# Kernel tuning notes

Hardware: AMD Instinct MI355X
Metric: run time of the kernel (lower is better)

## Reference

```python
import jax, jax.numpy as jnp
import numpy as np

B, D, Q = 256, 2048, 880880
NUM_CLASSES = 1000
T_K = 10.0  # self.T_k


def setup_inputs() -> dict:
    key = jax.random.key(0)
    k1, k2, k3, k4, k5, k6 = jax.random.split(key, 6)
    return {
        "features": jax.random.normal(k1, (B, D), dtype=jnp.float32),
        "labels": jax.random.randint(k2, (B,), 0, NUM_CLASSES),
        "pred": jax.random.randint(k3, (B,), 0, NUM_CLASSES),
        "confidence": jax.random.uniform(k4, (B,), dtype=jnp.float32),
        "queue_mus": jax.random.normal(k5, (Q,), dtype=jnp.float32),
        "queue_sigmas": jax.random.uniform(k6, (Q,), dtype=jnp.float32),
    }


def reference(features, labels, pred, confidence, queue_mus, queue_sigmas):
    # Per-sample feature statistics (torch.std is unbiased -> ddof=1)
    means = jnp.mean(features, axis=1)              # [B]
    stds = jnp.std(features, axis=1, ddof=1)        # [B]
    # Broadcast pairwise 'Wasserstein' distance vs queue: [B, Q]
    wd = jnp.sqrt((means[:, None] - queue_mus[None, :]) ** 2
                  + (stds[:, None] - queue_sigmas[None, :]) ** 2)
    min_distances = jnp.min(wd, axis=1)             # [B]
    # T_scale == 0 branch: T = exp(-T_k * min_dist)
    T = jnp.exp(-T_K * min_distances)
    return T
```

## Files before the change

kernel.cpp:

```cpp
#include <hip/hip_runtime.h>
#include <math.h>

#define NB 256
#define ND 2048
#define T_K 10.0f
#define SCAN2_BLOCKS 512
#define LDSCAP 2048

__global__ __launch_bounds__(256) void stats_probe_kernel(const float* __restrict__ feat,
                                                          const float* __restrict__ mus,
                                                          const float* __restrict__ sigmas,
                                                          float* __restrict__ stats,
                                                          float* __restrict__ u0part,
                                                          int Q) {
    const int b    = blockIdx.x;
    const int tid  = threadIdx.x;
    const int lane = tid & 63, wid = tid >> 6;
    __shared__ float ls[4], lq[4];

    const float4* row = (const float4*)(feat + (size_t)b * ND);
    float sum = 0.f, sumsq = 0.f;
#pragma unroll
    for (int i = 0; i < 2; ++i) {
        float4 v = row[tid + i * 256];
        sum   += v.x + v.y + v.z + v.w;
        sumsq += v.x * v.x + v.y * v.y + v.z * v.z + v.w * v.w;
    }
#pragma unroll
    for (int off = 32; off > 0; off >>= 1) {
        sum   += __shfl_down(sum, off, 64);
        sumsq += __shfl_down(sumsq, off, 64);
    }
    if (lane == 0) { ls[wid] = sum; lq[wid] = sumsq; }
    __syncthreads();
    if (tid == 0) {
        float S  = ls[0] + ls[1] + ls[2] + ls[3];
        float Q2 = lq[0] + lq[1] + lq[2] + lq[3];
        float mean = S / (float)ND;
        float var  = (Q2 - S * mean) / (float)(ND - 1);
        var = fmaxf(var, 0.f);
        stats[b]      = mean;
        stats[NB + b] = sqrtf(var);
    }

    const int nquad = Q >> 2;
    const int chunk = (nquad + NB - 1) / NB;
    const int qs    = b * chunk;
    const int qe    = min(qs + chunk, nquad);
    const float4* mu4 = (const float4*)mus;
    const float4* sg4 = (const float4*)sigmas;

    float best = INFINITY;
    for (int i = qs + tid; i < qe; i += 256) {
        float4 mu = mu4[i], sg = sg4[i];
        float s0 = sg.x - 1.f, s1 = sg.y - 1.f, s2e = sg.z - 1.f, s3 = sg.w - 1.f;
        best = fminf(best, fmaf(mu.x, mu.x, s0 * s0));
        best = fminf(best, fmaf(mu.y, mu.y, s1 * s1));
        best = fminf(best, fmaf(mu.z, mu.z, s2e * s2e));
        best = fminf(best, fmaf(mu.w, mu.w, s3 * s3));
    }
    if (b == 0) {
        int q = nquad * 4 + tid;
        if (q < Q) {
            float dm = mus[q], ds = sigmas[q] - 1.f;
            best = fminf(best, fmaf(dm, dm, ds * ds));
        }
    }
#pragma unroll
    for (int off = 32; off > 0; off >>= 1)
        best = fminf(best, __shfl_down(best, off, 64));
    __syncthreads();
    if (lane == 0) ls[wid] = best;
    __syncthreads();
    if (tid == 0)
        u0part[b] = fminf(fminf(ls[0], ls[1]), fminf(ls[2], ls[3]));
}

__global__ __launch_bounds__(256) void scan_filtered_kernel(const float* __restrict__ mus,
                                                            const float* __restrict__ sigmas,
                                                            const float* __restrict__ stats,
                                                            const float* __restrict__ u0part,
                                                            float* __restrict__ partial,
                                                            int Q) {
    const int tid  = threadIdx.x;
    const int lane = tid & 63, wid = tid >> 6;

    __shared__ float2 buf[LDSCAP];
    __shared__ float  red[4][NB];
    __shared__ float  ls[4], lq[4];
    __shared__ int    cnt;

    float u = u0part[tid];
    float mb = stats[tid], sb = stats[NB + tid];
    float dsb = sb - 1.f;
    float r2 = fmaf(mb, mb, dsb * dsb);
#pragma unroll
    for (int off = 32; off > 0; off >>= 1) {
        u  = fminf(u,  __shfl_down(u,  off, 64));
        r2 = fmaxf(r2, __shfl_down(r2, off, 64));
    }
    if (lane == 0) { ls[wid] = u; lq[wid] = r2; }
    if (tid == 0) cnt = 0;
    __syncthreads();
    const float U0  = fminf(fminf(ls[0], ls[1]), fminf(ls[2], ls[3]));
    const float R2  = fmaxf(fmaxf(lq[0], lq[1]), fmaxf(lq[2], lq[3]));
    const float thr = sqrtf(U0) + 2.f * sqrtf(R2);
    const float thr2 = thr * thr * 1.0001f + 1e-12f;

    float m2[4], s2[4];
#pragma unroll
    for (int k = 0; k < 4; ++k) {
        m2[k] = -2.f * stats[lane + 64 * k];
        s2[k] = -2.f * stats[NB + lane + 64 * k];
    }
    float acc[4];
#pragma unroll
    for (int k = 0; k < 4; ++k) acc[k] = INFINITY;

    const int nquad = Q >> 2;
    const float4* mu4 = (const float4*)mus;
    const float4* sg4 = (const float4*)sigmas;

    for (int cb = blockIdx.x * 256; cb < nquad; cb += SCAN2_BLOCKS * 256) {
        __syncthreads();
        if (cnt > LDSCAP - 1024) {
            const int n = cnt;
            for (int j = wid; j < n; j += 4) {
                float2 p = buf[j];
                float r = fmaf(p.x, p.x, p.y * p.y);
#pragma unroll
                for (int k = 0; k < 4; ++k)
                    acc[k] = fminf(acc[k], fmaf(m2[k], p.x, fmaf(s2[k], p.y, r)));
            }
            __syncthreads();
            if (tid == 0) cnt = 0;
            __syncthreads();
        }
        const int i = cb + tid;
        if (i < nquad) {
            float4 mu = mu4[i], sg = sg4[i];
#define TESTK(MX, SX)                                                        \
            {                                                                \
                float dm = (MX), dss = (SX) - 1.f;                           \
                float dd = fmaf(dm, dm, dss * dss);                          \
                if (dd <= thr2) {                                            \
                    int p = atomicAdd(&cnt, 1);                              \
                    buf[p] = make_float2((MX), (SX));                        \
                }                                                            \
            }
            TESTK(mu.x, sg.x)
            TESTK(mu.y, sg.y)
            TESTK(mu.z, sg.z)
            TESTK(mu.w, sg.w)
        }
    }
    if (blockIdx.x == 0) {
        int q = nquad * 4 + tid;
        if (q < Q) { TESTK(mus[q], sigmas[q]) }
    }
#undef TESTK

    __syncthreads();
    {
        const int n = cnt;
        for (int j = wid; j < n; j += 4) {
            float2 p = buf[j];
            float r = fmaf(p.x, p.x, p.y * p.y);
#pragma unroll
            for (int k = 0; k < 4; ++k)
                acc[k] = fminf(acc[k], fmaf(m2[k], p.x, fmaf(s2[k], p.y, r)));
        }
    }

    __syncthreads();
#pragma unroll
    for (int k = 0; k < 4; ++k) red[wid][lane + 64 * k] = acc[k];
    __syncthreads();
    float v = fminf(fminf(red[0][tid], red[1][tid]), fminf(red[2][tid], red[3][tid]));
    v = v + fmaf(mb, mb, sb * sb);
    partial[(size_t)blockIdx.x * NB + tid] = fmaxf(v, 0.f);
}

__global__ __launch_bounds__(256) void reduce_kernel(const float* __restrict__ partial,
                                                     float* __restrict__ out,
                                                     int nblocks) {
    const int b   = blockIdx.x;
    const int tid = threadIdx.x;
    float v = INFINITY;
    for (int i = tid; i < nblocks; i += 256)
        v = fminf(v, partial[(size_t)i * NB + b]);
#pragma unroll
    for (int off = 32; off > 0; off >>= 1)
        v = fminf(v, __shfl_down(v, off, 64));
    __shared__ float w[4];
    const int lane = tid & 63, wid = tid >> 6;
    if (lane == 0) w[wid] = v;
    __syncthreads();
    if (tid == 0) {
        float m = fminf(fminf(w[0], w[1]), fminf(w[2], w[3]));
        out[b] = expf(-T_K * sqrtf(m));
    }
}

extern "C" void kernel_launch(void* const* d_in, const int* in_sizes, int n_in,
                              void* d_out, int out_size, void* d_ws, size_t ws_size,
                              hipStream_t stream) {
    const float* features = (const float*)d_in[0];
    const float* queue_mus    = (const float*)d_in[4];
    const float* queue_sigmas = (const float*)d_in[5];
    const int Q = in_sizes[4];

    float* stats   = (float*)d_ws;
    float* u0part  = stats + 2 * NB;
    float* partial = u0part + NB;

    stats_probe_kernel<<<NB, 256, 0, stream>>>(features, queue_mus, queue_sigmas,
                                               stats, u0part, Q);
    scan_filtered_kernel<<<SCAN2_BLOCKS, 256, 0, stream>>>(queue_mus, queue_sigmas,
                                                           stats, u0part, partial, Q);
    reduce_kernel<<<NB, 256, 0, stream>>>(partial, (float*)d_out, SCAN2_BLOCKS);
}
```

Before: 17.40 us.

## Fuse queue probe into pruned scan using per-block local bound

The per-sample stats computation moves into its own kernel. The queue probe (nearest distance to the point (0,1)) now runs inside the scan kernel, so each block derives its pruning threshold from the minimum over its own chunk instead of a global minimum. Each block therefore re-reads its contiguous chunk right after probing it, likely from cache, rather than the whole queue being streamed twice across two kernels. The partial buffer shrinks to 256 entries, so the final reduction loads once per thread without looping. The trade-off is a looser per-block threshold, which may let more candidates through to the LDS buffer.

```diff
diff --git a/kernel.cpp b/kernel.cpp
--- a/kernel.cpp
+++ b/kernel.cpp
@@ -4,44 +4,53 @@
 #define NB 256
 #define ND 2048
 #define T_K 10.0f
-#define SCAN2_BLOCKS 512
 #define LDSCAP 2048
 
-__global__ __launch_bounds__(256) void stats_probe_kernel(const float* __restrict__ feat,
-                                                          const float* __restrict__ mus,
+__global__ __launch_bounds__(256) void stats_kernel(const float* __restrict__ feat,
+                                                    float* __restrict__ stats) {
+    const int b   = blockIdx.x;
+    const int tid = threadIdx.x;
+    const int lane = tid & 63, wid = tid >> 6;
+    __shared__ float ls[4], lq[4];
+
+    const float4* row = (const float4*)(feat + (size_t)b * ND);
+    float sum = 0.f, sumsq = 0.f;
+#pragma unroll
+    for (int i = 0; i < 2; ++i) {
+        float4 v = row[tid + i * 256];
+        sum   += v.x + v.y + v.z + v.w;
+        sumsq += v.x * v.x + v.y * v.y + v.z * v.z + v.w * v.w;
+    }
+#pragma unroll
+    for (int off = 32; off > 0; off >>= 1) {
+        sum   += __shfl_down(sum, off, 64);
+        sumsq += __shfl_down(sumsq, off, 64);
+    }
+    if (lane == 0) { ls[wid] = sum; lq[wid] = sumsq; }
+    __syncthreads();
+    if (tid == 0) {
+        float S  = ls[0] + ls[1] + ls[2] + ls[3];
+        float Q2 = lq[0] + lq[1] + lq[2] + lq[3];
+        float mean = S / (float)ND;
+        float var  = fmaxf((Q2 - S * mean) / (float)(ND - 1), 0.f);
+        stats[b]      = mean;
+        stats[NB + b] = sqrtf(var);
+    }
+}
+
+__global__ __launch_bounds__(256) void scan_pruned_kernel(const float* __restrict__ mus,
                                                           const float* __restrict__ sigmas,
-                                                          float* __restrict__ stats,
-                                                          float* __restrict__ u0part,
+                                                          const float* __restrict__ stats,
+                                                          float* __restrict__ partial,
                                                           int Q) {
     const int b    = blockIdx.x;
     const int tid  = threadIdx.x;
     const int lane = tid & 63, wid = tid >> 6;
-    __shared__ float ls[4], lq[4];
-
-    const float4* row = (const float4*)(feat + (size_t)b * ND);
-    float sum = 0.f, sumsq = 0.f;
-#pragma unroll
-    for (int i = 0; i < 2; ++i) {
-        float4 v = row[tid + i * 256];
-        sum   += v.x + v.y + v.z + v.w;
-        sumsq += v.x * v.x + v.y * v.y + v.z * v.z + v.w * v.w;
-    }
-#pragma unroll
-    for (int off = 32; off > 0; off >>= 1) {
-        sum   += __shfl_down(sum, off, 64);
-        sumsq += __shfl_down(sumsq, off, 64);
-    }
-    if (lane == 0) { ls[wid] = sum; lq[wid] = sumsq; }
-    __syncthreads();
-    if (tid == 0) {
-        float S  = ls[0] + ls[1] + ls[2] + ls[3];
-        float Q2 = lq[0] + lq[1] + lq[2] + lq[3];
-        float mean = S / (float)ND;
-        float var  = (Q2 - S * mean) / (float)(ND - 1);
-        var = fmaxf(var, 0.f);
-        stats[b]      = mean;
-        stats[NB + b] = sqrtf(var);
-    }
+
+    __shared__ float2 buf[LDSCAP];
+    __shared__ float  red[4][NB];
+    __shared__ float  ls[4], lq[4];
+    __shared__ int    cnt;
 
     const int nquad = Q >> 2;
     const int chunk = (nquad + NB - 1) / NB;
@@ -66,45 +75,23 @@
             best = fminf(best, fmaf(dm, dm, ds * ds));
         }
     }
-#pragma unroll
-    for (int off = 32; off > 0; off >>= 1)
-        best = fminf(best, __shfl_down(best, off, 64));
-    __syncthreads();
-    if (lane == 0) ls[wid] = best;
-    __syncthreads();
-    if (tid == 0)
-        u0part[b] = fminf(fminf(ls[0], ls[1]), fminf(ls[2], ls[3]));
-}
-
-__global__ __launch_bounds__(256) void scan_filtered_kernel(const float* __restrict__ mus,
-                                                            const float* __restrict__ sigmas,
-                                                            const float* __restrict__ stats,
-                                                            const float* __restrict__ u0part,
-                                                            float* __restrict__ partial,
-                                                            int Q) {
-    const int tid  = threadIdx.x;
-    const int lane = tid & 63, wid = tid >> 6;
-
-    __shared__ float2 buf[LDSCAP];
-    __shared__ float  red[4][NB];
-    __shared__ float  ls[4], lq[4];
-    __shared__ int    cnt;
-
-    float u = u0part[tid];
-    float mb = stats[tid], sb = stats[NB + tid];
-    float dsb = sb - 1.f;
-    float r2 = fmaf(mb, mb, dsb * dsb);
-#pragma unroll
-    for (int off = 32; off > 0; off >>= 1) {
-        u  = fminf(u,  __shfl_down(u,  off, 64));
-        r2 = fmaxf(r2, __shfl_down(r2, off, 64));
-    }
-    if (lane == 0) { ls[wid] = u; lq[wid] = r2; }
-    if (tid == 0) cnt = 0;
-    __syncthreads();
-    const float U0  = fminf(fminf(ls[0], ls[1]), fminf(ls[2], ls[3]));
-    const float R2  = fmaxf(fmaxf(lq[0], lq[1]), fmaxf(lq[2], lq[3]));
-    const float thr = sqrtf(U0) + 2.f * sqrtf(R2);
+
+    const float mb = stats[tid], sb = stats[NB + tid];
+    {
+        float dsb = sb - 1.f;
+        float r2 = fmaf(mb, mb, dsb * dsb);
+#pragma unroll
+        for (int off = 32; off > 0; off >>= 1) {
+            best = fminf(best, __shfl_down(best, off, 64));
+            r2   = fmaxf(r2,   __shfl_down(r2,   off, 64));
+        }
+        if (lane == 0) { ls[wid] = best; lq[wid] = r2; }
+        if (tid == 0) cnt = 0;
+    }
+    __syncthreads();
+    const float U0   = fminf(fminf(ls[0], ls[1]), fminf(ls[2], ls[3]));
+    const float R2   = fmaxf(fmaxf(lq[0], lq[1]), fmaxf(lq[2], lq[3]));
+    const float thr  = sqrtf(U0) + 2.f * sqrtf(R2);
     const float thr2 = thr * thr * 1.0001f + 1e-12f;
 
     float m2[4], s2[4];
@@ -117,11 +104,7 @@
 #pragma unroll
     for (int k = 0; k < 4; ++k) acc[k] = INFINITY;
 
-    const int nquad = Q >> 2;
-    const float4* mu4 = (const float4*)mus;
-    const float4* sg4 = (const float4*)sigmas;
-
-    for (int cb = blockIdx.x * 256; cb < nquad; cb += SCAN2_BLOCKS * 256) {
+    for (int base = qs; base < qe; base += 256) {
         __syncthreads();
         if (cnt > LDSCAP - 1024) {
             const int n = cnt;
@@ -136,8 +119,8 @@
             if (tid == 0) cnt = 0;
             __syncthreads();
         }
-        const int i = cb + tid;
-        if (i < nquad) {
+        const int i = base + tid;
+        if (i < qe) {
             float4 mu = mu4[i], sg = sg4[i];
 #define TESTK(MX, SX)                                                        \
             {                                                                \
@@ -154,7 +137,7 @@
             TESTK(mu.w, sg.w)
         }
     }
-    if (blockIdx.x == 0) {
+    if (b == 0) {
         int q = nquad * 4 + tid;
         if (q < Q) { TESTK(mus[q], sigmas[q]) }
     }
@@ -176,24 +159,23 @@
 #pragma unroll
     for (int k = 0; k < 4; ++k) red[wid][lane + 64 * k] = acc[k];
     __syncthreads();
-    float v = fminf(fminf(red[0][tid], red[1][tid]), fminf(red[2][tid], red[3][tid]));
-    v = v + fmaf(mb, mb, sb * sb);
-    partial[(size_t)blockIdx.x * NB + tid] = fmaxf(v, 0.f);
+    {
+        float v = fminf(fminf(red[0][tid], red[1][tid]), fminf(red[2][tid], red[3][tid]));
+        v = v + fmaf(mb, mb, sb * sb);
+        partial[(size_t)b * NB + tid] = fmaxf(v, 0.f);
+    }
 }
 
 __global__ __launch_bounds__(256) void reduce_kernel(const float* __restrict__ partial,
-                                                     float* __restrict__ out,
-                                                     int nblocks) {
+                                                     float* __restrict__ out) {
     const int b   = blockIdx.x;
     const int tid = threadIdx.x;
-    float v = INFINITY;
-    for (int i = tid; i < nblocks; i += 256)
-        v = fminf(v, partial[(size_t)i * NB + b]);
+    const int lane = tid & 63, wid = tid >> 6;
+    float v = partial[(size_t)tid * NB + b];
 #pragma unroll
     for (int off = 32; off > 0; off >>= 1)
         v = fminf(v, __shfl_down(v, off, 64));
     __shared__ float w[4];
-    const int lane = tid & 63, wid = tid >> 6;
     if (lane == 0) w[wid] = v;
     __syncthreads();
     if (tid == 0) {
@@ -211,12 +193,10 @@
     const int Q = in_sizes[4];
 
     float* stats   = (float*)d_ws;
-    float* u0part  = stats + 2 * NB;
-    float* partial = u0part + NB;
-
-    stats_probe_kernel<<<NB, 256, 0, stream>>>(features, queue_mus, queue_sigmas,
-                                               stats, u0part, Q);
-    scan_filtered_kernel<<<SCAN2_BLOCKS, 256, 0, stream>>>(queue_mus, queue_sigmas,
-                                                           stats, u0part, partial, Q);
-    reduce_kernel<<<NB, 256, 0, stream>>>(partial, (float*)d_out, SCAN2_BLOCKS);
-}
+    float* partial = stats + 2 * NB;
+
+    stats_kernel<<<NB, 256, 0, stream>>>(features, stats);
+    scan_pruned_kernel<<<NB, 256, 0, stream>>>(queue_mus, queue_sigmas, stats,
+                                               partial, Q);
+    reduce_kernel<<<NB, 256, 0, stream>>>(partial, (float*)d_out);
+}
```

New measurement: 19.09 us. +9.8%, slower.
